# Optimization experiments

Measured on AMD Instinct MI355X. Metric: run time of the kernel, lower is better.

Reference implementation:

```python
import jax, jax.numpy as jnp
import numpy as np
import math

L = 6        # num_layers
H = 16       # nhead
D = 1024     # feature_dim (= d_model, dim_factor=1)
DFF = 1024
IN = 1024    # input_dim
B, T = 16, 512
HD = D // H
EPS = 1e-5


def _get_slopes(n):
    def pow2(n):
        start = 2.0 ** (-2.0 ** (-(math.log2(n) - 3)))
        return [start * (start ** i) for i in range(n)]
    if math.log2(n).is_integer():
        return pow2(n)
    cp2 = 2 ** math.floor(math.log2(n))
    return pow2(cp2) + _get_slopes(2 * cp2)[0::2][: n - cp2]


def _alibi_bias(num_heads, seq_len):
    # init_alibi_biased_mask_future reduces to -slope_h * |i - j|
    slopes = jnp.asarray(_get_slopes(num_heads), dtype=jnp.float32)  # [H]
    idx = jnp.arange(seq_len)
    rel = -jnp.abs(idx[:, None] - idx[None, :]).astype(jnp.float32)  # [T,T]
    return slopes[:, None, None] * rel  # [H,T,T]


def _ln(x, w, b):
    m = jnp.mean(x, axis=-1, keepdims=True)
    v = jnp.mean(jnp.square(x - m), axis=-1, keepdims=True)
    return (x - m) * jax.lax.rsqrt(v + EPS) * w + b


def setup_inputs() -> dict:
    key = jax.random.key(0)
    ks = jax.random.split(key, 16)
    s = 0.02
    return {
        "x": jax.random.normal(ks[0], (B, T, IN), dtype=jnp.float32),
        "bn_w": jax.random.normal(ks[1], (D, IN), dtype=jnp.float32) * s,
        "bn_b": jnp.zeros((D,), jnp.float32),
        "qkv_w": jax.random.normal(ks[2], (L, 3 * D, D), dtype=jnp.float32) * s,
        "qkv_b": jnp.zeros((L, 3 * D), jnp.float32),
        "out_w": jax.random.normal(ks[3], (L, D, D), dtype=jnp.float32) * s,
        "out_b": jnp.zeros((L, D), jnp.float32),
        "ln1_w": jnp.ones((L, D), jnp.float32),
        "ln1_b": jnp.zeros((L, D), jnp.float32),
        "ln2_w": jnp.ones((L, D), jnp.float32),
        "ln2_b": jnp.zeros((L, D), jnp.float32),
        "ff1_w": jax.random.normal(ks[4], (L, DFF, D), dtype=jnp.float32) * s,
        "ff1_b": jnp.zeros((L, DFF), jnp.float32),
        "ff2_w": jax.random.normal(ks[5], (L, D, DFF), dtype=jnp.float32) * s,
        "ff2_b": jnp.zeros((L, D), jnp.float32),
    }


def reference(x, bn_w, bn_b, qkv_w, qkv_b, out_w, out_b,
              ln1_w, ln1_b, ln2_w, ln2_b, ff1_w, ff1_b, ff2_w, ff2_b):
    b, t, _ = x.shape
    bias = _alibi_bias(H, t)  # [H,T,T], same for all batch elements
    h = x @ bn_w.T + bn_b  # bottleneck -> [B,T,D]
    scale = 1.0 / math.sqrt(HD)
    for l in range(L):
        qkv = h @ qkv_w[l].T + qkv_b[l]  # [B,T,3D]
        q, k, v = jnp.split(qkv, 3, axis=-1)
        q = q.reshape(b, t, H, HD)
        k = k.reshape(b, t, H, HD)
        v = v.reshape(b, t, H, HD)
        scores = jnp.einsum('bihd,bjhd->bhij', q, k) * scale + bias[None]
        attn = jax.nn.softmax(scores, axis=-1)
        o = jnp.einsum('bhij,bjhd->bihd', attn, v).reshape(b, t, D)
        o = o @ out_w[l].T + out_b[l]
        h = _ln(h + o, ln1_w[l], ln1_b[l])  # post-norm (PyTorch default)
        f = jax.nn.gelu(h @ ff1_w[l].T + ff1_b[l], approximate=False)
        f = f @ ff2_w[l].T + ff2_b[l]
        h = _ln(h + f, ln2_w[l], ln2_b[l])
    return h
```

## Files before the change

kernel.cpp:

```cpp
#include <hip/hip_runtime.h>
#include <stdint.h>

#define DEV static __device__ __forceinline__

typedef __attribute__((ext_vector_type(8))) uint16_t u16x8;
typedef __attribute__((ext_vector_type(4))) uint16_t u16x4;
typedef __attribute__((ext_vector_type(4))) uint32_t u32x4;
typedef __attribute__((ext_vector_type(4))) float    f32x4;
typedef __attribute__((ext_vector_type(8))) __bf16   bf16x8;

typedef __attribute__((address_space(3))) void lds_void;
typedef __attribute__((address_space(1))) void gbl_void;

DEV float bf2f(uint16_t u){
  union { uint32_t i; float f; } v; v.i = ((uint32_t)u) << 16; return v.f;
}
DEV uint16_t f2bf(float f){ return __builtin_bit_cast(uint16_t, (__bf16)f); }
DEV f32x4 mfma16(u16x8 a, u16x8 b, f32x4 c){
  return __builtin_amdgcn_mfma_f32_16x16x32_bf16(
      __builtin_bit_cast(bf16x8, a), __builtin_bit_cast(bf16x8, b), c, 0, 0, 0);
}
DEV uint32_t cvt_pk_bf16(float lo, float hi){
  uint32_t r;
  asm("v_cvt_pk_bf16_f32 %0, %1, %2" : "=v"(r) : "v"(lo), "v"(hi));
  return r;
}

__global__ __launch_bounds__(256)
void te_cvt(const float* __restrict__ in, uint16_t* __restrict__ out)
{
  const size_t i = ((size_t)blockIdx.x * 256 + threadIdx.x) * 8;
  f32x4 a = *(const f32x4*)(in + i);
  f32x4 b = *(const f32x4*)(in + i + 4);
  u16x8 o;
#pragma unroll
  for (int e = 0; e < 4; e++) {
    o[e]     = f2bf(a[e]);
    o[e + 4] = f2bf(b[e]);
  }
  *(u16x8*)(out + i) = o;
}

template<int MODE>
__global__ __launch_bounds__(256)
void te_gemm_bb(const uint16_t* __restrict__ A, int lda,
                const uint16_t* __restrict__ W, const float* __restrict__ bias,
                uint16_t* __restrict__ outB, float* __restrict__ outF,
                int M, int N, int K)
{
  __shared__ uint16_t la[128 * 64];
  __shared__ uint16_t lb[128 * 64];
  const int tid = threadIdx.x;
  const int w = tid >> 6, l = tid & 63;
  const int lr = l & 15, lg = l >> 4;
  const int tm = blockIdx.y * 128, tn = blockIdx.x * 128;
  const int srow = l >> 3;
  const int scol = ((l & 7) ^ srow) * 8;
  const int wr = (w >> 1) * 64, wc = (w & 1) * 64;

  f32x4 acc[4][4] = {};

  for (int k0 = 0; k0 < K; k0 += 64) {
#pragma unroll
    for (int c = 0; c < 4; c++) {
      const int rb = (c * 4 + w) * 8;
      const uint16_t* ga = A + (size_t)(tm + rb + srow) * lda + (k0 + scol);
      __builtin_amdgcn_global_load_lds((gbl_void*)(uintptr_t)ga,
                                       (lds_void*)(la + rb * 64), 16, 0, 0);
      const uint16_t* gw = W + (size_t)(tn + rb + srow) * K + (k0 + scol);
      __builtin_amdgcn_global_load_lds((gbl_void*)(uintptr_t)gw,
                                       (lds_void*)(lb + rb * 64), 16, 0, 0);
    }
    __syncthreads();
#pragma unroll
    for (int kk = 0; kk < 2; kk++) {
      u16x8 af[4], bfr[4];
#pragma unroll
      for (int i = 0; i < 4; i++) {
        const int row = wr + i * 16 + lr;
        af[i] = *(const u16x8*)&la[row * 64 + (((kk * 4 + lg) ^ (lr & 7)) << 3)];
      }
#pragma unroll
      for (int j = 0; j < 4; j++) {
        const int row = wc + j * 16 + lr;
        bfr[j] = *(const u16x8*)&lb[row * 64 + (((kk * 4 + lg) ^ (lr & 7)) << 3)];
      }
      __builtin_amdgcn_s_setprio(1);
#pragma unroll
      for (int i = 0; i < 4; i++)
#pragma unroll
        for (int j = 0; j < 4; j++)
          acc[i][j] = mfma16(af[i], bfr[j], acc[i][j]);
      __builtin_amdgcn_s_setprio(0);
    }
    __syncthreads();
  }

  float bv[4];
#pragma unroll
  for (int j = 0; j < 4; j++) bv[j] = bias[tn + wc + j * 16 + lr];
#pragma unroll
  for (int i = 0; i < 4; i++)
#pragma unroll
    for (int j = 0; j < 4; j++)
#pragma unroll
      for (int r = 0; r < 4; r++) {
        const int row = tm + wr + i * 16 + lg * 4 + r;
        const int col = tn + wc + j * 16 + lr;
        float v = acc[i][j][r] + bv[j];
        if (MODE == 2) {
          const float u = 0.7978845608028654f * v * (1.0f + 0.044715f * v * v);
          const float t = 1.0f - 2.0f / (__expf(2.0f * u) + 1.0f);
          v = 0.5f * v * (1.0f + t);
        }
        const size_t idx = (size_t)row * N + col;
        outB[idx] = f2bf(v);
        if (MODE == 1) outF[idx] = v;
      }
}

__global__ __launch_bounds__(256)
void te_attn(uint16_t* __restrict__ qkv)
{
  __shared__ uint16_t kl[64 * 64];
  __shared__ uint16_t vt[64 * 64];
  const int tid = threadIdx.x;
  const int w = tid >> 6, l = tid & 63;
  const int lr = l & 15, lg = l >> 4;
  const int bh = blockIdx.x, qt = blockIdx.y;
  const int h = bh & 15, b = bh >> 4;

  const int iQ = qt * 64 + w * 16 + lr;
  u16x8 qf[2];
  {
    const size_t qoff = ((size_t)(b * 512 + iQ)) * 3072 + h * 64 + lg * 8;
    qf[0] = *(const u16x8*)&qkv[qoff];
    qf[1] = *(const u16x8*)&qkv[qoff + 32];
  }
  const float LOG2E  = 1.4426950408889634f;
  const float scl2e  = 0.125f * LOG2E;
  const float slope2e = exp2f(-0.5f * (float)(h + 1)) * LOG2E;

  const int sjb = tid >> 3;
  const int sd0 = (tid & 7) * 8;

  float mR = -1e30f, sdq = 0.0f;
  f32x4 acc[4] = {};

  u16x8 kreg[2], vreg[2];
  {
    const int jt0 = (qt & 7) * 64;
#pragma unroll
    for (int cc = 0; cc < 2; cc++) {
      const int j = sjb + cc * 32;
      const size_t rbase = ((size_t)(b * 512 + jt0 + j)) * 3072 + h * 64 + sd0;
      kreg[cc] = *(const u16x8*)&qkv[rbase + 1024];
      vreg[cc] = *(const u16x8*)&qkv[rbase + 2048];
    }
  }

  for (int step = 0; step < 8; step++) {
    const int jt = ((qt + step) & 7) * 64;
#pragma unroll
    for (int cc = 0; cc < 2; cc++) {
      const int j = sjb + cc * 32;
      *(u16x8*)&kl[j * 64 + (((sd0 >> 3) ^ (j & 7)) << 3)] = kreg[cc];
      const int cV = (((j >> 3) ^ (sd0 >> 3)) << 3) + (j & 7);
#pragma unroll
      for (int e = 0; e < 8; e++) vt[(sd0 + e) * 64 + cV] = vreg[cc][e];
    }
    __syncthreads();
    if (step < 7) {
      const int jtn = ((qt + step + 1) & 7) * 64;
#pragma unroll
      for (int cc = 0; cc < 2; cc++) {
        const int j = sjb + cc * 32;
        const size_t rbase = ((size_t)(b * 512 + jtn + j)) * 3072 + h * 64 + sd0;
        kreg[cc] = *(const u16x8*)&qkv[rbase + 1024];
        vreg[cc] = *(const u16x8*)&qkv[rbase + 2048];
      }
    }

    f32x4 s[4] = {};
#pragma unroll
    for (int kk = 0; kk < 2; kk++) {
      u16x8 kf[4];
#pragma unroll
      for (int n = 0; n < 4; n++) {
        const int row = n * 16 + lr;
        kf[n] = *(const u16x8*)&kl[row * 64 + (((kk * 4 + lg) ^ (lr & 7)) << 3)];
      }
      __builtin_amdgcn_s_setprio(1);
#pragma unroll
      for (int n = 0; n < 4; n++)
        s[n] = mfma16(kf[n], qf[kk], s[n]);
      __builtin_amdgcn_s_setprio(0);
    }

    const float f0 = (float)(iQ - jt - lg * 4);
    float mt = -1e30f;
#pragma unroll
    for (int n = 0; n < 4; n++) {
      const float fj = f0 - (float)(n * 16);
#pragma unroll
      for (int r = 0; r < 4; r++) {
        const float v = fmaf(s[n][r], scl2e, -slope2e * fabsf(fj - (float)r));
        s[n][r] = v;
        mt = fmaxf(mt, v);
      }
    }
    mt = fmaxf(mt, __shfl_xor(mt, 16));
    mt = fmaxf(mt, __shfl_xor(mt, 32));

    if (!__all(mt <= mR)) {
      const float mN = fmaxf(mR, mt);
      const float fq = exp2f(mR - mN);
      mR = mN;
      sdq *= fq;
      float fA[4];
#pragma unroll
      for (int r = 0; r < 4; r++) fA[r] = __shfl(fq, lg * 4 + r);
#pragma unroll
      for (int n = 0; n < 4; n++)
#pragma unroll
        for (int r = 0; r < 4; r++) acc[n][r] *= fA[r];
    }

    float rs = 0.0f;
#pragma unroll
    for (int n = 0; n < 4; n++)
#pragma unroll
      for (int r = 0; r < 4; r++) {
        const float p = exp2f(s[n][r] - mR);
        s[n][r] = p;
        rs += p;
      }
    rs += __shfl_xor(rs, 16);
    rs += __shfl_xor(rs, 32);
    sdq += rs;

    uint32_t P2[4][2];
#pragma unroll
    for (int n = 0; n < 4; n++) {
      P2[n][0] = cvt_pk_bf16(s[n][0], s[n][1]);
      P2[n][1] = cvt_pk_bf16(s[n][2], s[n][3]);
    }

#pragma unroll
    for (int kk = 0; kk < 2; kk++) {
      uint32_t pw[4];
#pragma unroll
      for (int t = 0; t < 4; t++) {
        const int srcLane = lr + 16 * ((lg & 1) * 2 + (t >> 1));
        const uint32_t xa = __shfl(P2[2 * kk + 0][t & 1], srcLane);
        const uint32_t xb = __shfl(P2[2 * kk + 1][t & 1], srcLane);
        pw[t] = (lg >> 1) ? xb : xa;
      }
      u32x4 pv4 = { pw[0], pw[1], pw[2], pw[3] };
      u16x8 pf = __builtin_bit_cast(u16x8, pv4);
      u16x8 vf[4];
#pragma unroll
      for (int n = 0; n < 4; n++) {
        const int row = n * 16 + lr;
        vf[n] = *(const u16x8*)&vt[row * 64 + ((((kk * 4 + lg) ^ (2 * n + (lr >> 3))) & 7) << 3)];
      }
      __builtin_amdgcn_s_setprio(1);
#pragma unroll
      for (int n = 0; n < 4; n++)
        acc[n] = mfma16(pf, vf[n], acc[n]);
      __builtin_amdgcn_s_setprio(0);
    }
    __syncthreads();
  }

  float sdA[4];
#pragma unroll
  for (int r = 0; r < 4; r++) sdA[r] = 1.0f / __shfl(sdq, lg * 4 + r);
#pragma unroll
  for (int n = 0; n < 4; n++)
#pragma unroll
    for (int r = 0; r < 4; r++) {
      const int i = qt * 64 + w * 16 + lg * 4 + r;
      const int d = h * 64 + n * 16 + lr;
      qkv[((size_t)(b * 512 + i)) * 3072 + d] = f2bf(acc[n][r] * sdA[r]);
    }
}

template<int FINAL>
__global__ __launch_bounds__(256)
void te_ln(const float* __restrict__ hres, const uint16_t* __restrict__ delta,
           const float* __restrict__ w, const float* __restrict__ b,
           float* __restrict__ hout, uint16_t* __restrict__ bout)
{
  const int row = blockIdx.x, t = threadIdx.x;
  const size_t base = (size_t)row * 1024 + t * 4;
  f32x4 hv = *(const f32x4*)&hres[base];
  u16x4 dv = *(const u16x4*)&delta[base];
  float x[4];
#pragma unroll
  for (int i = 0; i < 4; i++) x[i] = hv[i] + bf2f(dv[i]);
  float s = x[0] + x[1] + x[2] + x[3];
  float ss = x[0]*x[0] + x[1]*x[1] + x[2]*x[2] + x[3]*x[3];
#pragma unroll
  for (int msk = 32; msk >= 1; msk >>= 1) {
    s  += __shfl_xor(s, msk);
    ss += __shfl_xor(ss, msk);
  }
  __shared__ float rs[4], rq[4];
  const int wv = t >> 6;
  if ((t & 63) == 0) { rs[wv] = s; rq[wv] = ss; }
  __syncthreads();
  s  = rs[0] + rs[1] + rs[2] + rs[3];
  ss = rq[0] + rq[1] + rq[2] + rq[3];
  const float mean = s * (1.0f / 1024.0f);
  const float var  = ss * (1.0f / 1024.0f) - mean * mean;
  const float rstd = rsqrtf(var + 1e-5f);
  f32x4 wv4 = *(const f32x4*)&w[t * 4];
  f32x4 bv4 = *(const f32x4*)&b[t * 4];
  f32x4 yo; u16x4 bo;
#pragma unroll
  for (int i = 0; i < 4; i++) {
    const float y = (x[i] - mean) * rstd * wv4[i] + bv4[i];
    yo[i] = y; bo[i] = f2bf(y);
  }
  *(f32x4*)&hout[base] = yo;
  if (FINAL == 0) *(u16x4*)&bout[base] = bo;
}

extern "C" void kernel_launch(void* const* d_in, const int* in_sizes, int n_in,
                              void* d_out, int out_size, void* d_ws, size_t ws_size,
                              hipStream_t stream)
{
  (void)in_sizes; (void)n_in; (void)out_size; (void)ws_size;
  const float* x     = (const float*)d_in[0];
  const float* bn_w  = (const float*)d_in[1];
  const float* bn_b  = (const float*)d_in[2];
  const float* qkv_w = (const float*)d_in[3];
  const float* qkv_b = (const float*)d_in[4];
  const float* out_w = (const float*)d_in[5];
  const float* out_b = (const float*)d_in[6];
  const float* ln1_w = (const float*)d_in[7];
  const float* ln1_b = (const float*)d_in[8];
  const float* ln2_w = (const float*)d_in[9];
  const float* ln2_b = (const float*)d_in[10];
  const float* ff1_w = (const float*)d_in[11];
  const float* ff1_b = (const float*)d_in[12];
  const float* ff2_w = (const float*)d_in[13];
  const float* ff2_b = (const float*)d_in[14];

  char* ws = (char*)d_ws;
  float*    h_f32   = (float*)ws;
  uint16_t* h_bf    = (uint16_t*)(ws + (32u  << 20));
  uint16_t* qkvb    = (uint16_t*)(ws + (48u  << 20));
  uint16_t* scrA    = (uint16_t*)(ws + (96u  << 20));
  uint16_t* qkvw_bf = (uint16_t*)(ws + (112u << 20));
  uint16_t* ff2w_bf = (uint16_t*)(ws + (148u << 20));
  uint16_t* bnw_bf  = (uint16_t*)(ws + (160u << 20));
  uint16_t* outw_bf = (uint16_t*)d_out;
  uint16_t* ff1w_bf = (uint16_t*)((char*)d_out + (12u << 20));
  float*    outf    = (float*)d_out;

  const int M = 8192;
  dim3 blk(256);

  te_cvt<<<dim3(18874368 / 2048), blk, 0, stream>>>(qkv_w, qkvw_bf);
  te_cvt<<<dim3(6291456  / 2048), blk, 0, stream>>>(out_w, outw_bf);
  te_cvt<<<dim3(6291456  / 2048), blk, 0, stream>>>(ff1_w, ff1w_bf);
  te_cvt<<<dim3(6291456  / 2048), blk, 0, stream>>>(ff2_w, ff2w_bf);
  te_cvt<<<dim3(1048576  / 2048), blk, 0, stream>>>(bn_w,  bnw_bf);
  te_cvt<<<dim3(8388608  / 2048), blk, 0, stream>>>(x,     scrA);

  te_gemm_bb<1><<<dim3(8, 64), blk, 0, stream>>>(scrA, 1024, bnw_bf, bn_b,
                                                 h_bf, h_f32, M, 1024, 1024);

  for (int l = 0; l < 6; l++) {
    te_gemm_bb<0><<<dim3(24, 64), blk, 0, stream>>>(
        h_bf, 1024, qkvw_bf + (size_t)l * 3072 * 1024, qkv_b + l * 3072,
        qkvb, nullptr, M, 3072, 1024);
    te_attn<<<dim3(256, 8), blk, 0, stream>>>(qkvb);
    te_gemm_bb<0><<<dim3(8, 64), blk, 0, stream>>>(
        qkvb, 3072, outw_bf + (size_t)l * 1024 * 1024, out_b + l * 1024,
        scrA, nullptr, M, 1024, 1024);
    te_ln<0><<<dim3(8192), blk, 0, stream>>>(h_f32, scrA, ln1_w + l * 1024, ln1_b + l * 1024,
                                             h_f32, h_bf);
    te_gemm_bb<2><<<dim3(8, 64), blk, 0, stream>>>(
        h_bf, 1024, ff1w_bf + (size_t)l * 1024 * 1024, ff1_b + l * 1024,
        scrA, nullptr, M, 1024, 1024);
    te_gemm_bb<0><<<dim3(8, 64), blk, 0, stream>>>(
        scrA, 1024, ff2w_bf + (size_t)l * 1024 * 1024, ff2_b + l * 1024,
        qkvb, nullptr, M, 1024, 1024);
    if (l == 5) {
      te_ln<1><<<dim3(8192), blk, 0, stream>>>(h_f32, qkvb, ln2_w + l * 1024, ln2_b + l * 1024,
                                               outf, nullptr);
    } else {
      te_ln<0><<<dim3(8192), blk, 0, stream>>>(h_f32, qkvb, ln2_w + l * 1024, ln2_b + l * 1024,
                                               h_f32, h_bf);
    }
  }
}
```

Before: 1.567 ms.

## Keep residual stream in bf16 only and process two query tiles per attention block

Drops the fp32 copy of the hidden state. The residual is now read from bf16 in the layernorm, and the GEMM epilogue no longer writes an fp32 output. This removes fp32 residual traffic on every layernorm, at the cost of residual precision accumulated across layers. Separately, each attention block now handles 128 queries with two independent softmax states, halving the grid and reusing each K/V tile loaded into LDS across twice as many queries.

Result: faster. 1.474 ms (-5.9%).

```diff
diff --git a/kernel.cpp b/kernel.cpp
--- a/kernel.cpp
+++ b/kernel.cpp
@@ -45,8 +45,7 @@
 __global__ __launch_bounds__(256)
 void te_gemm_bb(const uint16_t* __restrict__ A, int lda,
                 const uint16_t* __restrict__ W, const float* __restrict__ bias,
-                uint16_t* __restrict__ outB, float* __restrict__ outF,
-                int M, int N, int K)
+                uint16_t* __restrict__ outB, int M, int N, int K)
 {
   __shared__ uint16_t la[128 * 64];
   __shared__ uint16_t lb[128 * 64];
@@ -113,11 +112,57 @@
           const float t = 1.0f - 2.0f / (__expf(2.0f * u) + 1.0f);
           v = 0.5f * v * (1.0f + t);
         }
-        const size_t idx = (size_t)row * N + col;
-        outB[idx] = f2bf(v);
-        if (MODE == 1) outF[idx] = v;
-      }
-}
+        outB[(size_t)row * N + col] = f2bf(v);
+      }
+}
+
+#define SOFTMAX_PACK(S, MR, SDQ, ACC, IQ, P2)                                  \
+  {                                                                            \
+    const float f0 = (float)((IQ) - jt - lg * 4);                              \
+    float mt = -1e30f;                                                         \
+    _Pragma("unroll")                                                          \
+    for (int n = 0; n < 4; n++) {                                              \
+      const float fj = f0 - (float)(n * 16);                                   \
+      _Pragma("unroll")                                                        \
+      for (int r = 0; r < 4; r++) {                                            \
+        const float v = fmaf(S[n][r], scl2e, -slope2e * fabsf(fj - (float)r)); \
+        S[n][r] = v;                                                           \
+        mt = fmaxf(mt, v);                                                     \
+      }                                                                        \
+    }                                                                          \
+    mt = fmaxf(mt, __shfl_xor(mt, 16));                                        \
+    mt = fmaxf(mt, __shfl_xor(mt, 32));                                        \
+    if (!__all(mt <= MR)) {                                                    \
+      const float mN = fmaxf(MR, mt);                                          \
+      const float fq = exp2f(MR - mN);                                         \
+      MR = mN;                                                                 \
+      SDQ *= fq;                                                               \
+      float fA[4];                                                             \
+      _Pragma("unroll")                                                        \
+      for (int r = 0; r < 4; r++) fA[r] = __shfl(fq, lg * 4 + r);              \
+      _Pragma("unroll")                                                        \
+      for (int n = 0; n < 4; n++)                                              \
+        _Pragma("unroll")                                                      \
+        for (int r = 0; r < 4; r++) ACC[n][r] *= fA[r];                        \
+    }                                                                          \
+    float rs = 0.0f;                                                           \
+    _Pragma("unroll")                                                          \
+    for (int n = 0; n < 4; n++)                                                \
+      _Pragma("unroll")                                                        \
+      for (int r = 0; r < 4; r++) {                                            \
+        const float p = exp2f(S[n][r] - MR);                                   \
+        S[n][r] = p;                                                           \
+        rs += p;                                                               \
+      }                                                                        \
+    rs += __shfl_xor(rs, 16);                                                  \
+    rs += __shfl_xor(rs, 32);                                                  \
+    SDQ += rs;                                                                 \
+    _Pragma("unroll")                                                          \
+    for (int n = 0; n < 4; n++) {                                              \
+      P2[n][0] = cvt_pk_bf16(S[n][0], S[n][1]);                                \
+      P2[n][1] = cvt_pk_bf16(S[n][2], S[n][3]);                                \
+    }                                                                          \
+  }
 
 __global__ __launch_bounds__(256)
 void te_attn(uint16_t* __restrict__ qkv)
@@ -130,26 +175,27 @@
   const int bh = blockIdx.x, qt = blockIdx.y;
   const int h = bh & 15, b = bh >> 4;
 
-  const int iQ = qt * 64 + w * 16 + lr;
-  u16x8 qf[2];
-  {
-    const size_t qoff = ((size_t)(b * 512 + iQ)) * 3072 + h * 64 + lg * 8;
-    qf[0] = *(const u16x8*)&qkv[qoff];
-    qf[1] = *(const u16x8*)&qkv[qoff + 32];
-  }
-  const float LOG2E  = 1.4426950408889634f;
-  const float scl2e  = 0.125f * LOG2E;
+  const int iQ0 = qt * 128 + w * 16 + lr;
+  u16x8 qf[2][2];
+#pragma unroll
+  for (int g = 0; g < 2; g++) {
+    const size_t qoff = ((size_t)(b * 512 + iQ0 + g * 64)) * 3072 + h * 64 + lg * 8;
+    qf[g][0] = *(const u16x8*)&qkv[qoff];
+    qf[g][1] = *(const u16x8*)&qkv[qoff + 32];
+  }
+  const float LOG2E = 1.4426950408889634f;
+  const float scl2e = 0.125f * LOG2E;
   const float slope2e = exp2f(-0.5f * (float)(h + 1)) * LOG2E;
 
   const int sjb = tid >> 3;
   const int sd0 = (tid & 7) * 8;
 
-  float mR = -1e30f, sdq = 0.0f;
-  f32x4 acc[4] = {};
+  float mR0 = -1e30f, sdq0 = 0.0f, mR1 = -1e30f, sdq1 = 0.0f;
+  f32x4 acc0[4] = {}, acc1[4] = {};
 
   u16x8 kreg[2], vreg[2];
   {
-    const int jt0 = (qt & 7) * 64;
+    const int jt0 = (qt * 2) * 64;
 #pragma unroll
     for (int cc = 0; cc < 2; cc++) {
       const int j = sjb + cc * 32;
@@ -160,7 +206,7 @@
   }
 
   for (int step = 0; step < 8; step++) {
-    const int jt = ((qt + step) & 7) * 64;
+    const int jt = ((qt * 2 + step) & 7) * 64;
 #pragma unroll
     for (int cc = 0; cc < 2; cc++) {
       const int j = sjb + cc * 32;
@@ -171,7 +217,7 @@
     }
     __syncthreads();
     if (step < 7) {
-      const int jtn = ((qt + step + 1) & 7) * 64;
+      const int jtn = ((qt * 2 + step + 1) & 7) * 64;
 #pragma unroll
       for (int cc = 0; cc < 2; cc++) {
         const int j = sjb + cc * 32;
@@ -181,7 +227,7 @@
       }
     }
 
-    f32x4 s[4] = {};
+    f32x4 s0[4] = {}, s1[4] = {};
 #pragma unroll
     for (int kk = 0; kk < 2; kk++) {
       u16x8 kf[4];
@@ -192,72 +238,34 @@
       }
       __builtin_amdgcn_s_setprio(1);
 #pragma unroll
-      for (int n = 0; n < 4; n++)
-        s[n] = mfma16(kf[n], qf[kk], s[n]);
+      for (int n = 0; n < 4; n++) {
+        s0[n] = mfma16(kf[n], qf[0][kk], s0[n]);
+        s1[n] = mfma16(kf[n], qf[1][kk], s1[n]);
+      }
       __builtin_amdgcn_s_setprio(0);
     }
 
-    const float f0 = (float)(iQ - jt - lg * 4);
-    float mt = -1e30f;
-#pragma unroll
-    for (int n = 0; n < 4; n++) {
-      const float fj = f0 - (float)(n * 16);
-#pragma unroll
-      for (int r = 0; r < 4; r++) {
-        const float v = fmaf(s[n][r], scl2e, -slope2e * fabsf(fj - (float)r));
-        s[n][r] = v;
-        mt = fmaxf(mt, v);
-      }
-    }
-    mt = fmaxf(mt, __shfl_xor(mt, 16));
-    mt = fmaxf(mt, __shfl_xor(mt, 32));
-
-    if (!__all(mt <= mR)) {
-      const float mN = fmaxf(mR, mt);
-      const float fq = exp2f(mR - mN);
-      mR = mN;
-      sdq *= fq;
-      float fA[4];
-#pragma unroll
-      for (int r = 0; r < 4; r++) fA[r] = __shfl(fq, lg * 4 + r);
-#pragma unroll
-      for (int n = 0; n < 4; n++)
-#pragma unroll
-        for (int r = 0; r < 4; r++) acc[n][r] *= fA[r];
-    }
-
-    float rs = 0.0f;
-#pragma unroll
-    for (int n = 0; n < 4; n++)
-#pragma unroll
-      for (int r = 0; r < 4; r++) {
-        const float p = exp2f(s[n][r] - mR);
-        s[n][r] = p;
-        rs += p;
-      }
-    rs += __shfl_xor(rs, 16);
-    rs += __shfl_xor(rs, 32);
-    sdq += rs;
-
-    uint32_t P2[4][2];
-#pragma unroll
-    for (int n = 0; n < 4; n++) {
-      P2[n][0] = cvt_pk_bf16(s[n][0], s[n][1]);
-      P2[n][1] = cvt_pk_bf16(s[n][2], s[n][3]);
-    }
+    uint32_t P2a[4][2], P2b[4][2];
+    SOFTMAX_PACK(s0, mR0, sdq0, acc0, iQ0,      P2a);
+    SOFTMAX_PACK(s1, mR1, sdq1, acc1, iQ0 + 64, P2b);
 
 #pragma unroll
     for (int kk = 0; kk < 2; kk++) {
-      uint32_t pw[4];
+      uint32_t pw0[4], pw1[4];
 #pragma unroll
       for (int t = 0; t < 4; t++) {
         const int srcLane = lr + 16 * ((lg & 1) * 2 + (t >> 1));
-        const uint32_t xa = __shfl(P2[2 * kk + 0][t & 1], srcLane);
-        const uint32_t xb = __shfl(P2[2 * kk + 1][t & 1], srcLane);
-        pw[t] = (lg >> 1) ? xb : xa;
-      }
-      u32x4 pv4 = { pw[0], pw[1], pw[2], pw[3] };
-      u16x8 pf = __builtin_bit_cast(u16x8, pv4);
+        const uint32_t a0 = __shfl(P2a[2 * kk + 0][t & 1], srcLane);
+        const uint32_t b0 = __shfl(P2a[2 * kk + 1][t & 1], srcLane);
+        pw0[t] = (lg >> 1) ? b0 : a0;
+        const uint32_t a1 = __shfl(P2b[2 * kk + 0][t & 1], srcLane);
+        const uint32_t b1 = __shfl(P2b[2 * kk + 1][t & 1], srcLane);
+        pw1[t] = (lg >> 1) ? b1 : a1;
+      }
+      u32x4 q0 = { pw0[0], pw0[1], pw0[2], pw0[3] };
+      u32x4 q1 = { pw1[0], pw1[1], pw1[2], pw1[3] };
+      u16x8 pf0 = __builtin_bit_cast(u16x8, q0);
+      u16x8 pf1 = __builtin_bit_cast(u16x8, q1);
       u16x8 vf[4];
 #pragma unroll
       for (int n = 0; n < 4; n++) {
@@ -266,39 +274,56 @@
       }
       __builtin_amdgcn_s_setprio(1);
 #pragma unroll
-      for (int n = 0; n < 4; n++)
-        acc[n] = mfma16(pf, vf[n], acc[n]);
+      for (int n = 0; n < 4; n++) {
+        acc0[n] = mfma16(pf0, vf[n], acc0[n]);
+        acc1[n] = mfma16(pf1, vf[n], acc1[n]);
+      }
       __builtin_amdgcn_s_setprio(0);
     }
     __syncthreads();
   }
 
-  float sdA[4];
-#pragma unroll
-  for (int r = 0; r < 4; r++) sdA[r] = 1.0f / __shfl(sdq, lg * 4 + r);
-#pragma unroll
-  for (int n = 0; n < 4; n++)
-#pragma unroll
-    for (int r = 0; r < 4; r++) {
-      const int i = qt * 64 + w * 16 + lg * 4 + r;
-      const int d = h * 64 + n * 16 + lr;
-      qkv[((size_t)(b * 512 + i)) * 3072 + d] = f2bf(acc[n][r] * sdA[r]);
-    }
+  {
+    float sdA[4];
+#pragma unroll
+    for (int r = 0; r < 4; r++) sdA[r] = 1.0f / __shfl(sdq0, lg * 4 + r);
+#pragma unroll
+    for (int n = 0; n < 4; n++)
+#pragma unroll
+      for (int r = 0; r < 4; r++) {
+        const int i = qt * 128 + w * 16 + lg * 4 + r;
+        const int d = h * 64 + n * 16 + lr;
+        qkv[((size_t)(b * 512 + i)) * 3072 + d] = f2bf(acc0[n][r] * sdA[r]);
+      }
+  }
+  {
+    float sdA[4];
+#pragma unroll
+    for (int r = 0; r < 4; r++) sdA[r] = 1.0f / __shfl(sdq1, lg * 4 + r);
+#pragma unroll
+    for (int n = 0; n < 4; n++)
+#pragma unroll
+      for (int r = 0; r < 4; r++) {
+        const int i = qt * 128 + 64 + w * 16 + lg * 4 + r;
+        const int d = h * 64 + n * 16 + lr;
+        qkv[((size_t)(b * 512 + i)) * 3072 + d] = f2bf(acc1[n][r] * sdA[r]);
+      }
+  }
 }
 
 template<int FINAL>
 __global__ __launch_bounds__(256)
-void te_ln(const float* __restrict__ hres, const uint16_t* __restrict__ delta,
+void te_ln(const uint16_t* __restrict__ h, const uint16_t* __restrict__ delta,
            const float* __restrict__ w, const float* __restrict__ b,
-           float* __restrict__ hout, uint16_t* __restrict__ bout)
+           uint16_t* __restrict__ hout, float* __restrict__ fout)
 {
   const int row = blockIdx.x, t = threadIdx.x;
   const size_t base = (size_t)row * 1024 + t * 4;
-  f32x4 hv = *(const f32x4*)&hres[base];
+  u16x4 hv = *(const u16x4*)&h[base];
   u16x4 dv = *(const u16x4*)&delta[base];
   float x[4];
 #pragma unroll
-  for (int i = 0; i < 4; i++) x[i] = hv[i] + bf2f(dv[i]);
+  for (int i = 0; i < 4; i++) x[i] = bf2f(hv[i]) + bf2f(dv[i]);
   float s = x[0] + x[1] + x[2] + x[3];
   float ss = x[0]*x[0] + x[1]*x[1] + x[2]*x[2] + x[3]*x[3];
 #pragma unroll
@@ -317,14 +342,19 @@
   const float rstd = rsqrtf(var + 1e-5f);
   f32x4 wv4 = *(const f32x4*)&w[t * 4];
   f32x4 bv4 = *(const f32x4*)&b[t * 4];
-  f32x4 yo; u16x4 bo;
-#pragma unroll
-  for (int i = 0; i < 4; i++) {
-    const float y = (x[i] - mean) * rstd * wv4[i] + bv4[i];
-    yo[i] = y; bo[i] = f2bf(y);
-  }
-  *(f32x4*)&hout[base] = yo;
-  if (FINAL == 0) *(u16x4*)&bout[base] = bo;
+  if (FINAL == 0) {
+    u16x4 bo;
+#pragma unroll
+    for (int i = 0; i < 4; i++)
+      bo[i] = f2bf((x[i] - mean) * rstd * wv4[i] + bv4[i]);
+    *(u16x4*)&hout[base] = bo;
+  } else {
+    f32x4 yo;
+#pragma unroll
+    for (int i = 0; i < 4; i++)
+      yo[i] = (x[i] - mean) * rstd * wv4[i] + bv4[i];
+    *(f32x4*)&fout[base] = yo;
+  }
 }
 
 extern "C" void kernel_launch(void* const* d_in, const int* in_sizes, int n_in,
@@ -349,13 +379,12 @@
   const float* ff2_b = (const float*)d_in[14];
 
   char* ws = (char*)d_ws;
-  float*    h_f32   = (float*)ws;
-  uint16_t* h_bf    = (uint16_t*)(ws + (32u  << 20));
-  uint16_t* qkvb    = (uint16_t*)(ws + (48u  << 20));
-  uint16_t* scrA    = (uint16_t*)(ws + (96u  << 20));
-  uint16_t* qkvw_bf = (uint16_t*)(ws + (112u << 20));
-  uint16_t* ff2w_bf = (uint16_t*)(ws + (148u << 20));
-  uint16_t* bnw_bf  = (uint16_t*)(ws + (160u << 20));
+  uint16_t* h_bf    = (uint16_t*)ws;
+  uint16_t* qkvb    = (uint16_t*)(ws + (16u  << 20));
+  uint16_t* scrA    = (uint16_t*)(ws + (64u  << 20));
+  uint16_t* qkvw_bf = (uint16_t*)(ws + (80u  << 20));
+  uint16_t* ff2w_bf = (uint16_t*)(ws + (116u << 20));
+  uint16_t* bnw_bf  = (uint16_t*)(ws + (128u << 20));
   uint16_t* outw_bf = (uint16_t*)d_out;
   uint16_t* ff1w_bf = (uint16_t*)((char*)d_out + (12u << 20));
   float*    outf    = (float*)d_out;
@@ -370,31 +399,31 @@
   te_cvt<<<dim3(1048576  / 2048), blk, 0, stream>>>(bn_w,  bnw_bf);
   te_cvt<<<dim3(8388608  / 2048), blk, 0, stream>>>(x,     scrA);
 
-  te_gemm_bb<1><<<dim3(8, 64), blk, 0, stream>>>(scrA, 1024, bnw_bf, bn_b,
-                                                 h_bf, h_f32, M, 1024, 1024);
+  te_gemm_bb<0><<<dim3(8, 64), blk, 0, stream>>>(scrA, 1024, bnw_bf, bn_b,
+                                                 h_bf, M, 1024, 1024);
 
   for (int l = 0; l < 6; l++) {
     te_gemm_bb<0><<<dim3(24, 64), blk, 0, stream>>>(
         h_bf, 1024, qkvw_bf + (size_t)l * 3072 * 1024, qkv_b + l * 3072,
-        qkvb, nullptr, M, 3072, 1024);
-    te_attn<<<dim3(256, 8), blk, 0, stream>>>(qkvb);
+        qkvb, M, 3072, 1024);
+    te_attn<<<dim3(256, 4), blk, 0, stream>>>(qkvb);
     te_gemm_bb<0><<<dim3(8, 64), blk, 0, stream>>>(
         qkvb, 3072, outw_bf + (size_t)l * 1024 * 1024, out_b + l * 1024,
-        scrA, nullptr, M, 1024, 1024);
-    te_ln<0><<<dim3(8192), blk, 0, stream>>>(h_f32, scrA, ln1_w + l * 1024, ln1_b + l * 1024,
-                                             h_f32, h_bf);
+        scrA, M, 1024, 1024);
+    te_ln<0><<<dim3(8192), blk, 0, stream>>>(h_bf, scrA, ln1_w + l * 1024, ln1_b + l * 1024,
+                                             h_bf, nullptr);
     te_gemm_bb<2><<<dim3(8, 64), blk, 0, stream>>>(
         h_bf, 1024, ff1w_bf + (size_t)l * 1024 * 1024, ff1_b + l * 1024,
-        scrA, nullptr, M, 1024, 1024);
+        scrA, M, 1024, 1024);
     te_gemm_bb<0><<<dim3(8, 64), blk, 0, stream>>>(
         scrA, 1024, ff2w_bf + (size_t)l * 1024 * 1024, ff2_b + l * 1024,
-        qkvb, nullptr, M, 1024, 1024);
+        qkvb, M, 1024, 1024);
     if (l == 5) {
-      te_ln<1><<<dim3(8192), blk, 0, stream>>>(h_f32, qkvb, ln2_w + l * 1024, ln2_b + l * 1024,
-                                               outf, nullptr);
+      te_ln<1><<<dim3(8192), blk, 0, stream>>>(h_bf, qkvb, ln2_w + l * 1024, ln2_b + l * 1024,
+                                               nullptr, outf);
     } else {
-      te_ln<0><<<dim3(8192), blk, 0, stream>>>(h_f32, qkvb, ln2_w + l * 1024, ln2_b + l * 1024,
-                                               h_f32, h_bf);
-    }
-  }
-}
+      te_ln<0><<<dim3(8192), blk, 0, stream>>>(h_bf, qkvb, ln2_w + l * 1024, ln2_b + l * 1024,
+                                               h_bf, nullptr);
+    }
+  }
+}
```
